# Performance work log

Hardware: AMD Instinct MI355X
Metric: run time of the kernel (lower is better)

## Reference

```python
import jax, jax.numpy as jnp
import numpy as np

KEEPRATE = 0.5


def setup_inputs() -> dict:
    key = jax.random.key(0)
    k1, k2, k3 = jax.random.split(key, 3)
    N, C, T, V, K = 64, 128, 256, 25, 3
    x = jax.random.normal(k1, (N, C, T, V), dtype=jnp.float32)
    A = jax.random.uniform(k2, (N, K, V, V), dtype=jnp.float32)
    p = jax.random.normal(k3, (C * T, 1), dtype=jnp.float32)
    return {"x": x, "A": A, "p": p}


def reference(x, A, p):
    N, C, T, V = x.shape
    Vk = int(KEEPRATE * V)  # number of joints kept
    # [N, V, C*T]
    xr = jnp.transpose(x.reshape(N, C * T, V), (0, 2, 1))
    # l2-normalized projection vector, score per node
    pn = p * jax.lax.rsqrt(jnp.sum(p * p))
    y = xr @ pn                       # [N, V, 1]
    ys = y[..., 0]                    # [N, V]
    idx = jnp.argsort(-ys, axis=-1)[:, :Vk]   # [N, Vk] top-k node indices
    y_hat = jax.nn.sigmoid(jnp.take_along_axis(ys, idx, axis=1))[..., None]  # [N, Vk, 1]
    xg = jnp.take_along_axis(xr, idx[..., None], axis=1) * y_hat             # [N, Vk, C*T]
    # adjacency squaring then row+col gather of kept nodes
    A2 = A @ A                        # [N, K, V, V]

    def _sel(a2, i):                  # a2: [K, V, V], i: [Vk]
        return a2[:, i][:, :, i]      # [K, Vk, Vk]

    A_out = jax.vmap(_sel)(A2, idx)   # [N, K, Vk, Vk]
    x_out = jnp.transpose(xg, (0, 2, 1)).reshape(N, C, T, Vk)
    return x_out, A_out
```

## Files before the change

### kernel.cpp

```cpp
#include <hip/hip_runtime.h>
#include <hip/hip_bf16.h>
#include <math.h>

constexpr int N  = 64;
constexpr int V  = 25;
constexpr int K  = 3;
constexpr int CT = 32768;
constexpr int VK = 12;
constexpr int SPLIT = 32;
constexpr int ROWS  = 256;
constexpr int CHUNK = CT / SPLIT;
constexpr int TILES = CHUNK / ROWS;
constexpr int NBLK_G = N * (CT / ROWS);

typedef float f32x4 __attribute__((ext_vector_type(4)));

constexpr size_t XC_OFF   = 212992;
constexpr size_t XC_BYTES = (size_t)N * V * CT * sizeof(ushort);

__device__ __forceinline__ float bf2f(ushort us) {
    return __uint_as_float((unsigned)us << 16);
}

__device__ __forceinline__ void gload_lds16(const float* g, float* l) {
    __builtin_amdgcn_global_load_lds(
        (const __attribute__((address_space(1))) void*)g,
        (__attribute__((address_space(3))) void*)l, 16, 0, 0);
}

__device__ __forceinline__ void stage_wave(const float* __restrict__ gsrc, float* ldsbuf,
                                           int wave, int lane) {
    const float* gw = gsrc + (size_t)wave * 1600;
    float* lw = ldsbuf + wave * 1600;
    #pragma unroll
    for (int i = 0; i < 6; ++i)
        gload_lds16(gw + (size_t)(i * 64 + lane) * 4, lw + i * 256);
    if (lane < 16)
        gload_lds16(gw + (size_t)(384 + lane) * 4, lw + 384 * 4);
}

template <bool WRITE_XC>
__global__ __launch_bounds__(256) void k_scores(const float* __restrict__ x,
                                                const float* __restrict__ p,
                                                float* __restrict__ partial_t,
                                                float* __restrict__ p2partial,
                                                ushort* __restrict__ xc) {
    const int n = blockIdx.x / SPLIT;
    const int s = blockIdx.x % SPLIT;
    const int ct0 = s * CHUNK;
    const float* xn = x + (size_t)n * CT * V;
    ushort* xcn = xc + (size_t)n * V * CT;
    const int tid = threadIdx.x, wave = tid >> 6, lane = tid & 63;

    __shared__ float lds[ROWS * V];

    float acc[V];
    #pragma unroll
    for (int v = 0; v < V; ++v) acc[v] = 0.f;
    float psq = 0.f;

    for (int tile = 0; tile < TILES; ++tile) {
        const int base_ct = ct0 + tile * ROWS;
        asm volatile("s_waitcnt lgkmcnt(0)" ::: "memory");
        stage_wave(xn + (size_t)base_ct * V, lds, wave, lane);
        asm volatile("s_waitcnt vmcnt(0)" ::: "memory");

        const float pv = p[base_ct + tid];
        psq += pv * pv;
        const float* row = lds + tid * V;
        #pragma unroll
        for (int v = 0; v < V; ++v) acc[v] += row[v] * pv;

        if (WRITE_XC) {
            const float* wrows = lds + wave * 64 * V;
            for (int pq = lane; pq < V * 8; pq += 64) {
                const int v     = pq >> 3;
                const int oct_l = pq & 7;
                const float* src = wrows + oct_l * 8 * V + v;
                unsigned u0, u1, u2, u3;
                asm("v_cvt_pk_bf16_f32 %0, %1, %2" : "=v"(u0) : "v"(src[0 * V]), "v"(src[1 * V]));
                asm("v_cvt_pk_bf16_f32 %0, %1, %2" : "=v"(u1) : "v"(src[2 * V]), "v"(src[3 * V]));
                asm("v_cvt_pk_bf16_f32 %0, %1, %2" : "=v"(u2) : "v"(src[4 * V]), "v"(src[5 * V]));
                asm("v_cvt_pk_bf16_f32 %0, %1, %2" : "=v"(u3) : "v"(src[6 * V]), "v"(src[7 * V]));
                uint4 pk = make_uint4(u0, u1, u2, u3);
                const int oct = wave * 8 + oct_l;
                *(uint4*)(xcn + (size_t)v * CT + base_ct + oct * 8) = pk;
            }
        }
    }

    #pragma unroll
    for (int v = 0; v < V; ++v) {
        float a = acc[v];
        #pragma unroll
        for (int off = 32; off > 0; off >>= 1) a += __shfl_down(a, off);
        acc[v] = a;
    }
    #pragma unroll
    for (int off = 32; off > 0; off >>= 1) psq += __shfl_down(psq, off);

    __shared__ float red[4][V];
    __shared__ float redp[4];
    if (lane == 0) {
        #pragma unroll
        for (int v = 0; v < V; ++v) red[wave][v] = acc[v];
        redp[wave] = psq;
    }
    __syncthreads();
    if (tid < V) {
        partial_t[((size_t)n * V + tid) * SPLIT + s] =
            red[0][tid] + red[1][tid] + red[2][tid] + red[3][tid];
    }
    if (tid == V && n == 0) {
        p2partial[s] = redp[0] + redp[1] + redp[2] + redp[3];
    }
}

__global__ __launch_bounds__(64) void k_topk(const float* __restrict__ partial_t,
                                             const float* __restrict__ p2partial,
                                             int* __restrict__ idxbuf,
                                             float* __restrict__ yhatbuf) {
    const int n = blockIdx.x, lane = threadIdx.x;
    float s2 = 0.f;
    #pragma unroll
    for (int i = 0; i < SPLIT; ++i) s2 += p2partial[i];

    float my = 0.f;
    if (lane < V) {
        const float4* pb = (const float4*)(partial_t + ((size_t)n * V + lane) * SPLIT);
        #pragma unroll
        for (int i = 0; i < SPLIT / 4; ++i) {
            float4 q = pb[i];
            my += q.x + q.y + q.z + q.w;
        }
    }
    int rank = 0;
    #pragma unroll
    for (int u = 0; u < V; ++u) {
        const float yu = __shfl(my, u);
        if (yu > my || (yu == my && u < lane)) ++rank;
    }
    if (lane < V && rank < VK) {
        idxbuf[n * VK + rank]  = lane;
        yhatbuf[n * VK + rank] = 1.0f / (1.0f + expf(-my * rsqrtf(s2)));
    }
}

__global__ __launch_bounds__(256) void k_gather_xc(const ushort* __restrict__ xc,
                                                   const float* __restrict__ A,
                                                   const int* __restrict__ idxbuf,
                                                   const float* __restrict__ yhatbuf,
                                                   float* __restrict__ xout,
                                                   float* __restrict__ aout) {
    __shared__ int   sidx[VK];
    __shared__ float syh[VK];
    const int tid = threadIdx.x, wave = tid >> 6, lane = tid & 63;

    if (blockIdx.x < (unsigned)NBLK_G) {
        const int n  = blockIdx.x >> 7;
        const int r0 = (blockIdx.x & 127) << 8;
        if (tid < VK) {
            sidx[tid] = idxbuf[n * VK + tid];
            syh[tid]  = yhatbuf[n * VK + tid];
        }
        __syncthreads();

        const ushort* xcn = xc + (size_t)n * V * CT + r0;
        f32x4* dst = (f32x4*)(xout + ((size_t)n * CT + r0) * VK);
        #pragma unroll
        for (int j = 0; j < 3; ++j) {
            const int f   = tid + j * 256;
            const int row = f / 3;
            const int c0  = (f % 3) * 4;
            f32x4 o;
            o.x = bf2f(xcn[(size_t)sidx[c0 + 0] * CT + row]) * syh[c0 + 0];
            o.y = bf2f(xcn[(size_t)sidx[c0 + 1] * CT + row]) * syh[c0 + 1];
            o.z = bf2f(xcn[(size_t)sidx[c0 + 2] * CT + row]) * syh[c0 + 2];
            o.w = bf2f(xcn[(size_t)sidx[c0 + 3] * CT + row]) * syh[c0 + 3];
            __builtin_nontemporal_store(o, &dst[f]);
        }
    } else {
        if (wave != 0) return;
        __shared__ float ldsA[V * V];
        const int b2 = blockIdx.x - NBLK_G;
        const int n  = b2 / K;
        const int k  = b2 % K;
        if (lane < VK) sidx[lane] = idxbuf[n * VK + lane];
        const float* Ak = A + ((size_t)n * K + k) * V * V;
        for (int i = lane; i < V * V; i += 64) ldsA[i] = Ak[i];
        asm volatile("s_waitcnt vmcnt(0) lgkmcnt(0)" ::: "memory");
        for (int o = lane; o < VK * VK; o += 64) {
            const int a  = o / VK, bc = o % VK;
            const int ia = sidx[a], ib = sidx[bc];
            float ssum = 0.f;
            #pragma unroll
            for (int m = 0; m < V; ++m) ssum += ldsA[ia * V + m] * ldsA[m * V + ib];
            __builtin_nontemporal_store(ssum, &aout[((size_t)n * K + k) * VK * VK + o]);
        }
    }
}

__global__ __launch_bounds__(256) void k_gather_aout(const float* __restrict__ x,
                                                     const float* __restrict__ A,
                                                     const int* __restrict__ idxbuf,
                                                     const float* __restrict__ yhatbuf,
                                                     float* __restrict__ xout,
                                                     float* __restrict__ aout) {
    __shared__ float lds[ROWS * V];
    __shared__ int   swidx[4][VK];
    __shared__ float swyh[4][VK];
    const int tid = threadIdx.x, wave = tid >> 6, lane = tid & 63;

    if (blockIdx.x < (unsigned)NBLK_G) {
        const int n  = blockIdx.x >> 7;
        const int r0 = (blockIdx.x & 127) << 8;
        stage_wave(x + ((size_t)n * CT + r0) * V, lds, wave, lane);
        if (lane < VK) {
            swidx[wave][lane] = idxbuf[n * VK + lane];
            swyh[wave][lane]  = yhatbuf[n * VK + lane];
        }
        asm volatile("s_waitcnt vmcnt(0) lgkmcnt(0)" ::: "memory");
        f32x4* dst = (f32x4*)(xout + ((size_t)n * CT + r0) * VK);
        #pragma unroll
        for (int j = 0; j < 3; ++j) {
            const int f   = 192 * wave + 64 * j + lane;
            const int row = f / 3;
            const int c0  = (f % 3) * 4;
            f32x4 o;
            o.x = lds[row * V + swidx[wave][c0 + 0]] * swyh[wave][c0 + 0];
            o.y = lds[row * V + swidx[wave][c0 + 1]] * swyh[wave][c0 + 1];
            o.z = lds[row * V + swidx[wave][c0 + 2]] * swyh[wave][c0 + 2];
            o.w = lds[row * V + swidx[wave][c0 + 3]] * swyh[wave][c0 + 3];
            __builtin_nontemporal_store(o, &dst[f]);
        }
    } else {
        if (wave != 0) return;
        const int b2 = blockIdx.x - NBLK_G;
        const int n  = b2 / K;
        const int k  = b2 % K;
        if (lane < VK) swidx[0][lane] = idxbuf[n * VK + lane];
        const float* Ak = A + ((size_t)n * K + k) * V * V;
        for (int i = lane; i < V * V; i += 64) lds[i] = Ak[i];
        asm volatile("s_waitcnt vmcnt(0) lgkmcnt(0)" ::: "memory");
        for (int o = lane; o < VK * VK; o += 64) {
            const int a  = o / VK, bc = o % VK;
            const int ia = swidx[0][a], ib = swidx[0][bc];
            float ssum = 0.f;
            #pragma unroll
            for (int m = 0; m < V; ++m) ssum += lds[ia * V + m] * lds[m * V + ib];
            __builtin_nontemporal_store(ssum, &aout[((size_t)n * K + k) * VK * VK + o]);
        }
    }
}

extern "C" void kernel_launch(void* const* d_in, const int* in_sizes, int n_in,
                              void* d_out, int out_size, void* d_ws, size_t ws_size,
                              hipStream_t stream) {
    const float* x = (const float*)d_in[0];
    const float* A = (const float*)d_in[1];
    const float* p = (const float*)d_in[2];

    float* xout = (float*)d_out;
    float* aout = xout + (size_t)N * CT * VK;

    char* ws = (char*)d_ws;
    float* partial_t = (float*)(ws);
    float* p2partial = (float*)(ws + 204800);
    float* yhatbuf   = (float*)(ws + 204928);
    int*   idxbuf    = (int*)  (ws + 208000);
    ushort* xc       = (ushort*)(ws + XC_OFF);

    const bool use_xc = ws_size >= XC_OFF + XC_BYTES;

    if (use_xc) {
        k_scores<true><<<N * SPLIT, 256, 0, stream>>>(x, p, partial_t, p2partial, xc);
        k_topk<<<N, 64, 0, stream>>>(partial_t, p2partial, idxbuf, yhatbuf);
        k_gather_xc<<<NBLK_G + N * K, 256, 0, stream>>>(xc, A, idxbuf, yhatbuf, xout, aout);
    } else {
        k_scores<false><<<N * SPLIT, 256, 0, stream>>>(x, p, partial_t, p2partial, xc);
        k_topk<<<N, 64, 0, stream>>>(partial_t, p2partial, idxbuf, yhatbuf);
        k_gather_aout<<<NBLK_G + N * K, 256, 0, stream>>>(x, A, idxbuf, yhatbuf, xout, aout);
    }
}
```

Baseline: 100.9 us.

## Stage bf16 copy in LDS per chunk and gather contiguous joint rows

The scores kernel now uses twice as many splits. Each block builds its bf16 transposed chunk in shared memory and writes it out as one contiguous block with nontemporal stores, instead of scattered 16-byte stores per tile. The gather kernel works per chunk: it loads the 12 selected joint rows directly into LDS with global_load_lds, then writes the output from LDS. This replaces strided per-element global reads. It adds a large shared-memory footprint (about 25KB in scores), which may reduce occupancy, and the k_topk loop that reads partial_t must match the new SPLIT.

```diff
diff --git a/kernel.cpp b/kernel.cpp
--- a/kernel.cpp
+++ b/kernel.cpp
@@ -7,15 +7,17 @@
 constexpr int K  = 3;
 constexpr int CT = 32768;
 constexpr int VK = 12;
-constexpr int SPLIT = 32;
+constexpr int SPLIT = 64;
+constexpr int CHUNK = CT / SPLIT;
 constexpr int ROWS  = 256;
-constexpr int CHUNK = CT / SPLIT;
 constexpr int TILES = CHUNK / ROWS;
-constexpr int NBLK_G = N * (CT / ROWS);
-
-typedef float f32x4 __attribute__((ext_vector_type(4)));
-
-constexpr size_t XC_OFF   = 212992;
+constexpr int NBLK_X = N * SPLIT;
+constexpr int NBLK_G6 = N * (CT / ROWS);
+
+typedef float    f32x4 __attribute__((ext_vector_type(4)));
+typedef unsigned u32x4 __attribute__((ext_vector_type(4)));
+
+constexpr size_t XC_OFF   = 417792;
 constexpr size_t XC_BYTES = (size_t)N * V * CT * sizeof(ushort);
 
 __device__ __forceinline__ float bf2f(ushort us) {
@@ -45,22 +47,22 @@
                                                 float* __restrict__ partial_t,
                                                 float* __restrict__ p2partial,
                                                 ushort* __restrict__ xc) {
-    const int n = blockIdx.x / SPLIT;
-    const int s = blockIdx.x % SPLIT;
+    const int n = blockIdx.x >> 6;
+    const int s = blockIdx.x & 63;
     const int ct0 = s * CHUNK;
     const float* xn = x + (size_t)n * CT * V;
-    ushort* xcn = xc + (size_t)n * V * CT;
     const int tid = threadIdx.x, wave = tid >> 6, lane = tid & 63;
 
-    __shared__ float lds[ROWS * V];
+    __shared__ __align__(16) float  lds[ROWS * V];
+    __shared__ __align__(16) ushort xcl[V * CHUNK];
 
     float acc[V];
     #pragma unroll
     for (int v = 0; v < V; ++v) acc[v] = 0.f;
     float psq = 0.f;
 
-    for (int tile = 0; tile < TILES; ++tile) {
-        const int base_ct = ct0 + tile * ROWS;
+    for (int t = 0; t < TILES; ++t) {
+        const int base_ct = ct0 + t * ROWS;
         asm volatile("s_waitcnt lgkmcnt(0)" ::: "memory");
         stage_wave(xn + (size_t)base_ct * V, lds, wave, lane);
         asm volatile("s_waitcnt vmcnt(0)" ::: "memory");
@@ -73,18 +75,20 @@
 
         if (WRITE_XC) {
             const float* wrows = lds + wave * 64 * V;
-            for (int pq = lane; pq < V * 8; pq += 64) {
-                const int v     = pq >> 3;
-                const int oct_l = pq & 7;
-                const float* src = wrows + oct_l * 8 * V + v;
-                unsigned u0, u1, u2, u3;
-                asm("v_cvt_pk_bf16_f32 %0, %1, %2" : "=v"(u0) : "v"(src[0 * V]), "v"(src[1 * V]));
-                asm("v_cvt_pk_bf16_f32 %0, %1, %2" : "=v"(u1) : "v"(src[2 * V]), "v"(src[3 * V]));
-                asm("v_cvt_pk_bf16_f32 %0, %1, %2" : "=v"(u2) : "v"(src[4 * V]), "v"(src[5 * V]));
-                asm("v_cvt_pk_bf16_f32 %0, %1, %2" : "=v"(u3) : "v"(src[6 * V]), "v"(src[7 * V]));
-                uint4 pk = make_uint4(u0, u1, u2, u3);
-                const int oct = wave * 8 + oct_l;
-                *(uint4*)(xcn + (size_t)v * CT + base_ct + oct * 8) = pk;
+            #pragma unroll
+            for (int it = 0; it < 4; ++it) {
+                const int pq = lane + it * 64;
+                if (pq < V * 8) {
+                    const int v = pq >> 3, o = pq & 7;
+                    const float* src = wrows + o * 8 * V + v;
+                    unsigned u0, u1, u2, u3;
+                    asm("v_cvt_pk_bf16_f32 %0, %1, %2" : "=v"(u0) : "v"(src[0 * V]), "v"(src[1 * V]));
+                    asm("v_cvt_pk_bf16_f32 %0, %1, %2" : "=v"(u1) : "v"(src[2 * V]), "v"(src[3 * V]));
+                    asm("v_cvt_pk_bf16_f32 %0, %1, %2" : "=v"(u2) : "v"(src[4 * V]), "v"(src[5 * V]));
+                    asm("v_cvt_pk_bf16_f32 %0, %1, %2" : "=v"(u3) : "v"(src[6 * V]), "v"(src[7 * V]));
+                    u32x4 pk = {u0, u1, u2, u3};
+                    *(u32x4*)(xcl + v * CHUNK + t * ROWS + wave * 64 + o * 8) = pk;
+                }
             }
         }
     }
@@ -107,12 +111,20 @@
         redp[wave] = psq;
     }
     __syncthreads();
+
     if (tid < V) {
         partial_t[((size_t)n * V + tid) * SPLIT + s] =
             red[0][tid] + red[1][tid] + red[2][tid] + red[3][tid];
     }
     if (tid == V && n == 0) {
         p2partial[s] = redp[0] + redp[1] + redp[2] + redp[3];
+    }
+
+    if (WRITE_XC) {
+        const u32x4* srcv = (const u32x4*)xcl;
+        u32x4* dstg = (u32x4*)(xc + (size_t)(n * SPLIT + s) * V * CHUNK);
+        for (int i = tid; i < V * CHUNK / 8; i += 256)
+            __builtin_nontemporal_store(srcv[i], &dstg[i]);
     }
 }
 
@@ -152,37 +164,43 @@
                                                    const float* __restrict__ yhatbuf,
                                                    float* __restrict__ xout,
                                                    float* __restrict__ aout) {
-    __shared__ int   sidx[VK];
+    const int tid = threadIdx.x, wave = tid >> 6, lane = tid & 63;
+    __shared__ __align__(16) ushort xl[VK * CHUNK];
     __shared__ float syh[VK];
-    const int tid = threadIdx.x, wave = tid >> 6, lane = tid & 63;
-
-    if (blockIdx.x < (unsigned)NBLK_G) {
-        const int n  = blockIdx.x >> 7;
-        const int r0 = (blockIdx.x & 127) << 8;
-        if (tid < VK) {
-            sidx[tid] = idxbuf[n * VK + tid];
-            syh[tid]  = yhatbuf[n * VK + tid];
-        }
+
+    if (blockIdx.x < (unsigned)NBLK_X) {
+        const int n = blockIdx.x >> 6, s = blockIdx.x & 63;
+        const ushort* xcs = xc + (size_t)(n * SPLIT + s) * V * CHUNK;
+
+        #pragma unroll
+        for (int jj = 0; jj < 3; ++jj) {
+            const int j  = wave * 3 + jj;
+            const int ia = __builtin_amdgcn_readfirstlane(idxbuf[n * VK + j]);
+            gload_lds16((const float*)(xcs + (size_t)ia * CHUNK + lane * 8),
+                        (float*)(xl + j * CHUNK));
+        }
+        if (tid < VK) syh[tid] = yhatbuf[n * VK + tid];
+        asm volatile("s_waitcnt vmcnt(0)" ::: "memory");
         __syncthreads();
 
-        const ushort* xcn = xc + (size_t)n * V * CT + r0;
-        f32x4* dst = (f32x4*)(xout + ((size_t)n * CT + r0) * VK);
-        #pragma unroll
-        for (int j = 0; j < 3; ++j) {
-            const int f   = tid + j * 256;
-            const int row = f / 3;
-            const int c0  = (f % 3) * 4;
+        f32x4* dst = (f32x4*)(xout + ((size_t)n * CT + s * CHUNK) * VK);
+        #pragma unroll
+        for (int jj = 0; jj < 6; ++jj) {
+            const int f  = tid + jj * 256;
+            const int ct = f / 3;
+            const int c0 = (f % 3) * 4;
             f32x4 o;
-            o.x = bf2f(xcn[(size_t)sidx[c0 + 0] * CT + row]) * syh[c0 + 0];
-            o.y = bf2f(xcn[(size_t)sidx[c0 + 1] * CT + row]) * syh[c0 + 1];
-            o.z = bf2f(xcn[(size_t)sidx[c0 + 2] * CT + row]) * syh[c0 + 2];
-            o.w = bf2f(xcn[(size_t)sidx[c0 + 3] * CT + row]) * syh[c0 + 3];
+            o.x = bf2f(xl[(c0 + 0) * CHUNK + ct]) * syh[c0 + 0];
+            o.y = bf2f(xl[(c0 + 1) * CHUNK + ct]) * syh[c0 + 1];
+            o.z = bf2f(xl[(c0 + 2) * CHUNK + ct]) * syh[c0 + 2];
+            o.w = bf2f(xl[(c0 + 3) * CHUNK + ct]) * syh[c0 + 3];
             __builtin_nontemporal_store(o, &dst[f]);
         }
     } else {
         if (wave != 0) return;
         __shared__ float ldsA[V * V];
-        const int b2 = blockIdx.x - NBLK_G;
+        __shared__ int   sidx[VK];
+        const int b2 = blockIdx.x - NBLK_X;
         const int n  = b2 / K;
         const int k  = b2 % K;
         if (lane < VK) sidx[lane] = idxbuf[n * VK + lane];
@@ -211,7 +229,7 @@
     __shared__ float swyh[4][VK];
     const int tid = threadIdx.x, wave = tid >> 6, lane = tid & 63;
 
-    if (blockIdx.x < (unsigned)NBLK_G) {
+    if (blockIdx.x < (unsigned)NBLK_G6) {
         const int n  = blockIdx.x >> 7;
         const int r0 = (blockIdx.x & 127) << 8;
         stage_wave(x + ((size_t)n * CT + r0) * V, lds, wave, lane);
@@ -235,7 +253,7 @@
         }
     } else {
         if (wave != 0) return;
-        const int b2 = blockIdx.x - NBLK_G;
+        const int b2 = blockIdx.x - NBLK_G6;
         const int n  = b2 / K;
         const int k  = b2 % K;
         if (lane < VK) swidx[0][lane] = idxbuf[n * VK + lane];
@@ -265,20 +283,20 @@
 
     char* ws = (char*)d_ws;
     float* partial_t = (float*)(ws);
-    float* p2partial = (float*)(ws + 204800);
-    float* yhatbuf   = (float*)(ws + 204928);
-    int*   idxbuf    = (int*)  (ws + 208000);
+    float* p2partial = (float*)(ws + 409600);
+    float* yhatbuf   = (float*)(ws + 409856);
+    int*   idxbuf    = (int*)  (ws + 412928);
     ushort* xc       = (ushort*)(ws + XC_OFF);
 
     const bool use_xc = ws_size >= XC_OFF + XC_BYTES;
 
     if (use_xc) {
-        k_scores<true><<<N * SPLIT, 256, 0, stream>>>(x, p, partial_t, p2partial, xc);
+        k_scores<true><<<NBLK_X, 256, 0, stream>>>(x, p, partial_t, p2partial, xc);
         k_topk<<<N, 64, 0, stream>>>(partial_t, p2partial, idxbuf, yhatbuf);
-        k_gather_xc<<<NBLK_G + N * K, 256, 0, stream>>>(xc, A, idxbuf, yhatbuf, xout, aout);
+        k_gather_xc<<<NBLK_X + N * K, 256, 0, stream>>>(xc, A, idxbuf, yhatbuf, xout, aout);
     } else {
-        k_scores<false><<<N * SPLIT, 256, 0, stream>>>(x, p, partial_t, p2partial, xc);
+        k_scores<false><<<NBLK_X, 256, 0, stream>>>(x, p, partial_t, p2partial, xc);
         k_topk<<<N, 64, 0, stream>>>(partial_t, p2partial, idxbuf, yhatbuf);
-        k_gather_aout<<<NBLK_G + N * K, 256, 0, stream>>>(x, A, idxbuf, yhatbuf, xout, aout);
-    }
-}
+        k_gather_aout<<<NBLK_G6 + N * K, 256, 0, stream>>>(x, A, idxbuf, yhatbuf, xout, aout);
+    }
+}
```

New measurement: 95.71 us. 5.1% less time.
